# Performance work log

Hardware: AMD Instinct MI355X
Metric: run time of the kernel (lower is better)

Reference implementation:

```python
import jax, jax.numpy as jnp
import numpy as np

RBF_START = 0.0
RBF_END = 10.0
RBF_STEPS = 32
OUT_SIZE = 64
ENERGY_SCALE = 1.0

L, R, T = 128, 1024, 16  # lig atoms, rec atoms, transform hypotheses


def setup_inputs() -> dict:
    key = jax.random.key(0)
    k1, k2, k3, k4 = jax.random.split(key, 4)
    return {
        "lig_feat": jax.random.normal(k1, (L, RBF_STEPS, OUT_SIZE), dtype=jnp.float32),
        "rec_feat": jax.random.normal(k2, (R, RBF_STEPS, OUT_SIZE), dtype=jnp.float32),
        "lig_coords": jax.random.normal(k3, (T, L, 3), dtype=jnp.float32),  # transformed lig coords per hypothesis
        "rec_coords": jax.random.normal(k4, (R, 3), dtype=jnp.float32),
    }


def reference(lig_feat, rec_feat, lig_coords, rec_coords):
    # attention coefficients: [L, R, E] where E = rbf_steps
    atn = jnp.einsum('lef,ref->lre', lig_feat, rec_feat)

    mu = jnp.linspace(RBF_START, RBF_END, RBF_STEPS, dtype=jnp.float32)  # [E]
    sigma = (RBF_START - RBF_END) / RBF_STEPS  # matches original (sign irrelevant, squared)

    # pairwise distances per transform: [T, L, R]
    diff = lig_coords[:, :, None, :] - rec_coords[None, None, :, :]  # [T, L, R, 3]
    dists = jnp.sqrt(jnp.sum(diff * diff, axis=-1))  # [T, L, R]

    # RBF encode: [T, L, R, E]
    rbf = jnp.exp(-(((dists[..., None] - mu) / sigma) ** 2))

    # attention-weighted energy reduction per transform: [T]
    Us = jnp.einsum('lre,tlre->t', atn, rbf) * ENERGY_SCALE
    return Us
```

## Files before the change

kernel.cpp:

```cpp
#include <hip/hip_runtime.h>
#include <hip/hip_bf16.h>

#define L_CNT 128
#define R_CNT 1024
#define T_CNT 16
#define E_CNT 32
#define F_CNT 64

constexpr float SFAC    = 3.8435917f;
constexpr float MUS     = SFAC * (10.0f / 31.0f);
constexpr float INV_MUS = 1.0f / MUS;

#if defined(__has_builtin)
#  if __has_builtin(__builtin_amdgcn_exp2f)
#    define EXP2(x) __builtin_amdgcn_exp2f(x)
#  endif
#endif
#ifndef EXP2
#  define EXP2(x) exp2f(x)
#endif

typedef __attribute__((ext_vector_type(8))) short short8_t;
typedef __attribute__((ext_vector_type(4))) float f32x4;

__device__ __forceinline__ short f2bf(float f) {
    __bf16 h = (__bf16)f;
    return __builtin_bit_cast(short, h);
}

#define PADK 72
__global__ __launch_bounds__(256) void atn_mfma(const float* __restrict__ lig,
                                                const float* __restrict__ rec,
                                                unsigned short* __restrict__ atn) {
    const int e   = blockIdx.x;
    const int l0  = blockIdx.y * 64;
    const int r0  = blockIdx.z * 128;
    const int tid = threadIdx.x;

    __shared__ __align__(16) short As[64 * PADK];
    __shared__ __align__(16) short Bs[128 * PADK];

#pragma unroll
    for (int i = 0; i < 4; ++i) {
        int idx = i * 256 + tid;
        int row = idx >> 4;
        int f4  = idx & 15;
        float4 v = *(const float4*)(lig + ((size_t)(l0 + row) * 32 + e) * 64 + f4 * 4);
        short4 p;
        p.x = f2bf(v.x); p.y = f2bf(v.y); p.z = f2bf(v.z); p.w = f2bf(v.w);
        *(short4*)(&As[row * PADK + f4 * 4]) = p;
    }
#pragma unroll
    for (int i = 0; i < 8; ++i) {
        int idx = i * 256 + tid;
        int row = idx >> 4;
        int f4  = idx & 15;
        float4 v = *(const float4*)(rec + ((size_t)(r0 + row) * 32 + e) * 64 + f4 * 4);
        short4 p;
        p.x = f2bf(v.x); p.y = f2bf(v.y); p.z = f2bf(v.z); p.w = f2bf(v.w);
        *(short4*)(&Bs[row * PADK + f4 * 4]) = p;
    }
    __syncthreads();

    const int wave = tid >> 6;
    const int lane = tid & 63;
    const int fr   = lane & 15;
    const int kg   = lane >> 4;

    f32x4 acc[8];
#pragma unroll
    for (int n = 0; n < 8; ++n) acc[n] = (f32x4){0.f, 0.f, 0.f, 0.f};

    short8_t a0 = *(short8_t*)(&As[(16 * wave + fr) * PADK + kg * 8]);
    short8_t a1 = *(short8_t*)(&As[(16 * wave + fr) * PADK + 32 + kg * 8]);

#pragma unroll
    for (int n = 0; n < 8; ++n) {
        short8_t b0 = *(short8_t*)(&Bs[(16 * n + fr) * PADK + kg * 8]);
        short8_t b1 = *(short8_t*)(&Bs[(16 * n + fr) * PADK + 32 + kg * 8]);
        acc[n] = __builtin_amdgcn_mfma_f32_16x16x32_bf16(a0, b0, acc[n], 0, 0, 0);
        acc[n] = __builtin_amdgcn_mfma_f32_16x16x32_bf16(a1, b1, acc[n], 0, 0, 0);
    }

    const int orow = l0 + 16 * wave + (lane >> 4) * 4;
    const int ocol = r0 + fr;
#pragma unroll
    for (int n = 0; n < 8; ++n) {
#pragma unroll
        for (int j = 0; j < 4; ++j) {
            size_t off = ((size_t)e * 128 + orow + j) * 1024 + ocol + 16 * n;
            atn[off] = (unsigned short)f2bf(acc[n][j]);
        }
    }
}

__global__ __launch_bounds__(256) void energy_kernel(const unsigned short* __restrict__ atn,
                                                     const float* __restrict__ ligc,
                                                     const float* __restrict__ recc,
                                                     float* __restrict__ partials) {
    __shared__ unsigned int atn_sd[E_CNT * 128];
    const unsigned short* atn_su = (const unsigned short*)atn_sd;

    const int tid   = threadIdx.x;
    const int l     = blockIdx.x >> 2;
    const int rbase = (blockIdx.x & 3) * 256;
    const int r     = rbase + tid;

    const unsigned int* atn_d = (const unsigned int*)atn;
    unsigned int stage[16];
#pragma unroll
    for (int it = 0; it < 16; ++it) {
        int idx = it * 256 + tid;
        int e   = idx >> 7;
        int rh  = idx & 127;
        stage[it] = atn_d[(size_t)e * 65536 + (size_t)l * 512 + (rbase >> 1) + rh];
    }

    const float rx = recc[r * 3 + 0];
    const float ry = recc[r * 3 + 1];
    const float rz = recc[r * 3 + 2];

    float d[T_CNT];
#pragma unroll
    for (int t = 0; t < T_CNT; ++t) {
        float dx = ligc[((size_t)t * 128 + l) * 3 + 0] - rx;
        float dy = ligc[((size_t)t * 128 + l) * 3 + 1] - ry;
        float dz = ligc[((size_t)t * 128 + l) * 3 + 2] - rz;
        d[t] = sqrtf(dx * dx + dy * dy + dz * dz);
    }

#pragma unroll
    for (int it = 0; it < 16; ++it) atn_sd[it * 256 + tid] = stage[it];
    __syncthreads();

    float acc[T_CNT];
#pragma unroll
    for (int t = 0; t < T_CNT; ++t) acc[t] = 0.0f;

#pragma unroll
    for (int t = 0; t < T_CNT; ++t) {
        const float u   = d[t] * SFAC;
        float e0f = rintf(u * INV_MUS);
        e0f = fminf(fmaxf(e0f, 3.0f), 28.0f);
        const int   em3 = (int)e0f - 3;
        const float um  = fmaf(e0f, -MUS, u);
#pragma unroll
        for (int k = 0; k < 7; ++k) {
            const float w  = um - (float)(k - 3) * MUS;
            const float ae = __uint_as_float((unsigned)atn_su[(em3 + k) * 256 + tid] << 16);
            acc[t] = fmaf(ae, EXP2(-(w * w)), acc[t]);
        }
    }

    __shared__ float red[4][T_CNT];
    const int lane = tid & 63;
    const int wid  = tid >> 6;
#pragma unroll
    for (int t = 0; t < T_CNT; ++t) {
#pragma unroll
        for (int m = 32; m >= 1; m >>= 1) acc[t] += __shfl_xor(acc[t], m, 64);
    }
    if (lane == 0) {
#pragma unroll
        for (int t = 0; t < T_CNT; ++t) red[wid][t] = acc[t];
    }
    __syncthreads();
    if (tid < T_CNT) {
        float s = red[0][tid] + red[1][tid] + red[2][tid] + red[3][tid];
        partials[(size_t)blockIdx.x * T_CNT + tid] = s;
    }
}

__global__ __launch_bounds__(256) void final_reduce(const float* __restrict__ partials,
                                                    float* __restrict__ out) {
    __shared__ float red[16][17];
    const int t = threadIdx.x & 15;
    const int g = threadIdx.x >> 4;
    float s = 0.0f;
    for (int b = g; b < 512; b += 16) s += partials[(size_t)b * 16 + t];
    red[g][t] = s;
    __syncthreads();
    if (threadIdx.x < 16) {
        float v = 0.0f;
#pragma unroll
        for (int g2 = 0; g2 < 16; ++g2) v += red[g2][threadIdx.x];
        out[threadIdx.x] = v;
    }
}

extern "C" void kernel_launch(void* const* d_in, const int* in_sizes, int n_in,
                              void* d_out, int out_size, void* d_ws, size_t ws_size,
                              hipStream_t stream) {
    const float* lig  = (const float*)d_in[0];
    const float* rec  = (const float*)d_in[1];
    const float* ligc = (const float*)d_in[2];
    const float* recc = (const float*)d_in[3];
    float* out = (float*)d_out;

    unsigned short* atn = (unsigned short*)d_ws;
    float* partials = (float*)((char*)d_ws + (size_t)E_CNT * L_CNT * R_CNT * 2);

    atn_mfma<<<dim3(E_CNT, 2, 8), 256, 0, stream>>>(lig, rec, atn);
    energy_kernel<<<512, 256, 0, stream>>>(atn, ligc, recc, partials);
    final_reduce<<<1, 256, 0, stream>>>(partials, out);
}
```

Before: 28.08 us.

## Fuse final reduction via fixed-point atomics, coalesce atn stores, narrow RBF window

Removes the third final_reduce launch: each energy block adds its per-transform sums to global 64-bit fixed-point accumulators, and the last block to finish writes the output. The atn GEMM output is now staged through swizzled shared memory so it can be written with 16-byte vector stores instead of scattered 2-byte stores. The RBF window shrinks from 7 to 5 neighbouring centers, which cuts exp and FMA work but drops more Gaussian tail contribution, so accuracy is lower. Fixed-point quantisation adds rounding error, and zeroing the accumulators from the first kernel creates an ordering dependency between the two launches.

```diff
diff --git a/kernel.cpp b/kernel.cpp
--- a/kernel.cpp
+++ b/kernel.cpp
@@ -5,11 +5,12 @@
 #define R_CNT 1024
 #define T_CNT 16
 #define E_CNT 32
-#define F_CNT 64
 
 constexpr float SFAC    = 3.8435917f;
 constexpr float MUS     = SFAC * (10.0f / 31.0f);
 constexpr float INV_MUS = 1.0f / MUS;
+constexpr float FIXSCALE = 2097152.0f;
+constexpr double INV_FIXSCALE = 1.0 / 2097152.0;
 
 #if defined(__has_builtin)
 #  if __has_builtin(__builtin_amdgcn_exp2f)
@@ -29,16 +30,23 @@
 }
 
 #define PADK 72
+#define CPAD 136
+
 __global__ __launch_bounds__(256) void atn_mfma(const float* __restrict__ lig,
                                                 const float* __restrict__ rec,
-                                                unsigned short* __restrict__ atn) {
+                                                unsigned short* __restrict__ atn,
+                                                unsigned long long* __restrict__ finals) {
     const int e   = blockIdx.x;
     const int l0  = blockIdx.y * 64;
     const int r0  = blockIdx.z * 128;
     const int tid = threadIdx.x;
 
-    __shared__ __align__(16) short As[64 * PADK];
-    __shared__ __align__(16) short Bs[128 * PADK];
+    if ((blockIdx.x | blockIdx.y | blockIdx.z) == 0 && tid < 17) finals[tid] = 0ULL;
+
+    __shared__ __align__(16) short smem[64 * PADK + 128 * PADK];
+    short* As = smem;
+    short* Bs = smem + 64 * PADK;
+    short* Cs = smem;
 
 #pragma unroll
     for (int i = 0; i < 4; ++i) {
@@ -81,25 +89,39 @@
         acc[n] = __builtin_amdgcn_mfma_f32_16x16x32_bf16(a0, b0, acc[n], 0, 0, 0);
         acc[n] = __builtin_amdgcn_mfma_f32_16x16x32_bf16(a1, b1, acc[n], 0, 0, 0);
     }
-
-    const int orow = l0 + 16 * wave + (lane >> 4) * 4;
-    const int ocol = r0 + fr;
+    __syncthreads();
+
+    const int orow_l = 16 * wave + (lane >> 4) * 4;
+    const int sw_w   = ((orow_l >> 2) & 3) << 4;
 #pragma unroll
     for (int n = 0; n < 8; ++n) {
 #pragma unroll
         for (int j = 0; j < 4; ++j) {
-            size_t off = ((size_t)e * 128 + orow + j) * 1024 + ocol + 16 * n;
-            atn[off] = (unsigned short)f2bf(acc[n][j]);
+            Cs[(orow_l + j) * CPAD + ((16 * n + fr) ^ sw_w)] = f2bf(acc[n][j]);
         }
+    }
+    __syncthreads();
+
+#pragma unroll
+    for (int it2 = 0; it2 < 4; ++it2) {
+        int idx = it2 * 256 + tid;
+        int row = idx >> 4;
+        int c8  = idx & 15;
+        int sw  = ((row >> 2) & 3) << 4;
+        short8_t v = *(short8_t*)(&Cs[row * CPAD + ((c8 * 8) ^ sw)]);
+        *(short8_t*)(&atn[((size_t)e * 128 + l0 + row) * 1024 + r0 + c8 * 8]) = v;
     }
 }
 
 __global__ __launch_bounds__(256) void energy_kernel(const unsigned short* __restrict__ atn,
                                                      const float* __restrict__ ligc,
                                                      const float* __restrict__ recc,
-                                                     float* __restrict__ partials) {
+                                                     unsigned long long* __restrict__ finals,
+                                                     float* __restrict__ out) {
     __shared__ unsigned int atn_sd[E_CNT * 128];
     const unsigned short* atn_su = (const unsigned short*)atn_sd;
+    __shared__ float red[4][T_CNT];
+    __shared__ unsigned int lastflag;
 
     const int tid   = threadIdx.x;
     const int l     = blockIdx.x >> 2;
@@ -111,9 +133,9 @@
 #pragma unroll
     for (int it = 0; it < 16; ++it) {
         int idx = it * 256 + tid;
-        int e   = idx >> 7;
+        int ee  = idx >> 7;
         int rh  = idx & 127;
-        stage[it] = atn_d[(size_t)e * 65536 + (size_t)l * 512 + (rbase >> 1) + rh];
+        stage[it] = atn_d[(size_t)ee * 65536 + (size_t)l * 512 + (rbase >> 1) + rh];
     }
 
     const float rx = recc[r * 3 + 0];
@@ -139,20 +161,19 @@
 
 #pragma unroll
     for (int t = 0; t < T_CNT; ++t) {
-        const float u   = d[t] * SFAC;
+        const float u = d[t] * SFAC;
         float e0f = rintf(u * INV_MUS);
-        e0f = fminf(fmaxf(e0f, 3.0f), 28.0f);
-        const int   em3 = (int)e0f - 3;
+        e0f = fminf(fmaxf(e0f, 2.0f), 29.0f);
+        const int   em2 = (int)e0f - 2;
         const float um  = fmaf(e0f, -MUS, u);
 #pragma unroll
-        for (int k = 0; k < 7; ++k) {
-            const float w  = um - (float)(k - 3) * MUS;
-            const float ae = __uint_as_float((unsigned)atn_su[(em3 + k) * 256 + tid] << 16);
+        for (int k = 0; k < 5; ++k) {
+            const float w  = um - (float)(k - 2) * MUS;
+            const float ae = __uint_as_float((unsigned)atn_su[(em2 + k) * 256 + tid] << 16);
             acc[t] = fmaf(ae, EXP2(-(w * w)), acc[t]);
         }
     }
 
-    __shared__ float red[4][T_CNT];
     const int lane = tid & 63;
     const int wid  = tid >> 6;
 #pragma unroll
@@ -165,26 +186,25 @@
         for (int t = 0; t < T_CNT; ++t) red[wid][t] = acc[t];
     }
     __syncthreads();
+
     if (tid < T_CNT) {
         float s = red[0][tid] + red[1][tid] + red[2][tid] + red[3][tid];
-        partials[(size_t)blockIdx.x * T_CNT + tid] = s;
-    }
-}
-
-__global__ __launch_bounds__(256) void final_reduce(const float* __restrict__ partials,
-                                                    float* __restrict__ out) {
-    __shared__ float red[16][17];
-    const int t = threadIdx.x & 15;
-    const int g = threadIdx.x >> 4;
-    float s = 0.0f;
-    for (int b = g; b < 512; b += 16) s += partials[(size_t)b * 16 + t];
-    red[g][t] = s;
-    __syncthreads();
-    if (threadIdx.x < 16) {
-        float v = 0.0f;
-#pragma unroll
-        for (int g2 = 0; g2 < 16; ++g2) v += red[g2][threadIdx.x];
-        out[threadIdx.x] = v;
+        long long q = (long long)llrintf(s * FIXSCALE);
+        atomicAdd(&finals[tid], (unsigned long long)q);
+    }
+    __threadfence();
+    __syncthreads();
+    if (tid == 0) {
+        unsigned long long old = atomicAdd(&finals[16], 1ULL);
+        lastflag = (old == 511ULL) ? 1u : 0u;
+    }
+    __syncthreads();
+    if (lastflag) {
+        __threadfence();
+        if (tid < T_CNT) {
+            unsigned long long v = atomicAdd(&finals[tid], 0ULL);
+            out[tid] = (float)((double)(long long)v * INV_FIXSCALE);
+        }
     }
 }
 
@@ -198,9 +218,9 @@
     float* out = (float*)d_out;
 
     unsigned short* atn = (unsigned short*)d_ws;
-    float* partials = (float*)((char*)d_ws + (size_t)E_CNT * L_CNT * R_CNT * 2);
-
-    atn_mfma<<<dim3(E_CNT, 2, 8), 256, 0, stream>>>(lig, rec, atn);
-    energy_kernel<<<512, 256, 0, stream>>>(atn, ligc, recc, partials);
-    final_reduce<<<1, 256, 0, stream>>>(partials, out);
-}
+    unsigned long long* finals =
+        (unsigned long long*)((char*)d_ws + (size_t)E_CNT * L_CNT * R_CNT * 2);
+
+    atn_mfma<<<dim3(E_CNT, 2, 8), 256, 0, stream>>>(lig, rec, atn, finals);
+    energy_kernel<<<512, 256, 0, stream>>>(atn, ligc, recc, finals, out);
+}
```

New measurement: 48.48 us. 72.6% more time.
